# Optimization experiments

Hardware: AMD Instinct MI355X
Metric: run time of the kernel (lower is better)

## Reference

```python
import jax, jax.numpy as jnp
import numpy as np
import math

B, D, E = 32768, 256, 8          # batch, feature dim (shape=[256]), num_steps experts
T_TOTAL = 1.0
H_STEP = T_TOTAL / E             # self.h
EIGMIN, EIGINIT, EIGMAX = -1.0, 0.0, 1.0
LOGIT_099 = math.log(0.99 / 0.01)


def setup_inputs() -> dict:
    key = jax.random.key(0)
    k_t, k_y, k_w1, k_w2 = jax.random.split(key, 4)
    std = 1.0 / math.sqrt(D)     # xavier-ish init for expert weights
    return {
        "t": jax.random.uniform(k_t, (B,), dtype=jnp.float32),            # times in [0, T)
        "y": jax.random.normal(k_y, (B, D), dtype=jnp.float32),
        "W1": jax.random.normal(k_w1, (E, D, D), dtype=jnp.float32) * std,
        "b1": jnp.zeros((E, D), dtype=jnp.float32),
        "W2": jax.random.normal(k_w2, (E, D, D), dtype=jnp.float32) * std,
        "b2": jnp.zeros((E, D), dtype=jnp.float32),
        "scales": jnp.full((1, D), LOGIT_099, dtype=jnp.float32),         # learn_scales=False init
        "shifta": jnp.asarray(LOGIT_099, dtype=jnp.float32),
        "shiftb": jnp.asarray(LOGIT_099, dtype=jnp.float32),
    }


def reference(t, y, W1, b1, W2, b2, scales, shifta, shiftb):
    # t2ind: clamp(int(t / h), max=E-1)
    ind = jnp.minimum((t / H_STEP).astype(jnp.int32), E - 1)            # [B]
    # per-sample dispatch to expert F[i] (2-layer MLP), grouped as masked
    # dense batched GEMMs per expert (E is a small fixed set)
    f = jnp.zeros_like(y)
    for e in range(E):
        h_e = jnp.tanh(jnp.einsum('bd,kd->bk', y, W1[e]) + b1[e])       # [B, D]
        f_e = jnp.einsum('bd,kd->bk', h_e, W2[e]) + b2[e]               # [B, D]
        f = jnp.where((ind == e)[:, None], f_e, f)
    # sigmoid-scale / affine-combine epilogue
    f = jax.nn.sigmoid(scales) * f
    a = EIGINIT + jax.nn.sigmoid(shifta) * (EIGMIN - EIGINIT)
    b = EIGINIT + jax.nn.sigmoid(shiftb) * (EIGMAX - EIGINIT)
    return 0.5 * ((b - a) * f + (a + b) * y)
```

## Files before the change

kernel.cpp:

```cpp
#include <hip/hip_runtime.h>

#define BATCH 32768
#define DIM   256
#define NEXP  8
#define MT    32
#define STRIDE 264

typedef __bf16 bf16x8 __attribute__((ext_vector_type(8)));
typedef __bf16 bf16x4 __attribute__((ext_vector_type(4)));
typedef float  f32x16 __attribute__((ext_vector_type(16)));

static __device__ __forceinline__ float sigmoid_f(float x) {
    return __builtin_amdgcn_rcpf(1.f + __expf(-x));
}
static __device__ __forceinline__ float tanh_f(float x) {
    return 1.f - 2.f * __builtin_amdgcn_rcpf(__expf(2.f * x) + 1.f);
}

static __device__ __forceinline__ void lds_barrier() {
    asm volatile("s_waitcnt lgkmcnt(0)\n\ts_barrier" ::: "memory");
}

__global__ void prep_kernel(const float* __restrict__ W1, const float* __restrict__ W2,
                            const float* __restrict__ t,
                            bf16x8* __restrict__ W1p, bf16x8* __restrict__ W2p,
                            int* __restrict__ cursor, int* __restrict__ idxb) {
    const int b = blockIdx.x;
    if (b < 256) {
        const int tid = b * 256 + threadIdx.x;
        const int kh  = tid & 1;
        const int ks  = (tid >> 1) & 15;
        const int col = (tid >> 5) & 255;
        const int e   = tid >> 13;
        const long src = (long)tid * 8;
        const float4 a0 = *(const float4*)(W1 + src);
        const float4 a1 = *(const float4*)(W1 + src + 4);
        const float4 c0 = *(const float4*)(W2 + src);
        const float4 c1 = *(const float4*)(W2 + src + 4);
        bf16x8 w1, w2;
        w1[0] = (__bf16)a0.x; w1[1] = (__bf16)a0.y; w1[2] = (__bf16)a0.z; w1[3] = (__bf16)a0.w;
        w1[4] = (__bf16)a1.x; w1[5] = (__bf16)a1.y; w1[6] = (__bf16)a1.z; w1[7] = (__bf16)a1.w;
        w2[0] = (__bf16)c0.x; w2[1] = (__bf16)c0.y; w2[2] = (__bf16)c0.z; w2[3] = (__bf16)c0.w;
        w2[4] = (__bf16)c1.x; w2[5] = (__bf16)c1.y; w2[6] = (__bf16)c1.z; w2[7] = (__bf16)c1.w;
        const int dst = (e << 13) | ((col >> 5) << 10) | (ks << 6) | (kh << 5) | (col & 31);
        W1p[dst] = w1;
        W2p[dst] = w2;
    } else {
        __shared__ int h[NEXP], base[NEXP];
        if (threadIdx.x < NEXP) h[threadIdx.x] = 0;
        __syncthreads();
        const int i = (b - 256) * 256 + threadIdx.x;
        const int e = min((int)(t[i] * 8.0f), NEXP - 1);
        const int lr = atomicAdd(&h[e], 1);
        __syncthreads();
        if (threadIdx.x < NEXP)
            base[threadIdx.x] = atomicAdd(&cursor[threadIdx.x], h[threadIdx.x]);
        __syncthreads();
        idxb[e * BATCH + base[e] + lr] = i;
    }
}

__global__ void __launch_bounds__(512, 2)
mlp_kernel(const float* __restrict__ y,
           const float* __restrict__ scales,
           const float* __restrict__ shifta,
           const float* __restrict__ shiftb,
           const float* __restrict__ b1,
           const float* __restrict__ b2,
           const bf16x8* __restrict__ W1p,
           const bf16x8* __restrict__ W2p,
           const int* __restrict__ cnt,
           const int* __restrict__ idxb,
           float* __restrict__ out) {
    __shared__ __bf16 Y[2][MT * STRIDE];
    __shared__ __bf16 H[2][MT * STRIDE];
    __shared__ int rowsb[4][MT];

    const int tx   = threadIdx.x;
    const int wave = tx >> 6;
    const int lane = tx & 63;
    const int nl   = lane & 31;
    const int kh   = lane >> 5;
    const bool isG1 = (wave < 4);
    const int  w    = wave & 3;
    const int  n0   = w * 64 + nl;
    const int  n1   = n0 + 32;

    const int e    = blockIdx.x >> 5;
    const int slot = blockIdx.x & 31;
    const int ce   = cnt[e];
    const int nt_e = (ce + MT - 1) >> 5;
    if (slot >= nt_e) return;
    const int nt   = ((nt_e - slot) + 31) >> 5;
    const int* idx_e = idxb + e * BATCH;

    const bf16x8* wp = (isG1 ? W1p : W2p) + (e << 13) + ((w * 2) << 10) + lane;
    bf16x8 wf[2][16];
#pragma unroll
    for (int s = 0; s < 2; ++s)
#pragma unroll
        for (int ks = 0; ks < 16; ++ks)
            wf[s][ks] = wp[(s << 10) + (ks << 6)];

    const float sa = sigmoid_f(shifta[0]);
    const float sb = sigmoid_f(shiftb[0]);
    const float k1 = 0.5f * (sb + sa);
    const float k2 = 0.5f * (sb - sa);
    const bool needy = (k2 != 0.0f);
    float b1v[2], b2v[2], cc[2];
    b1v[0] = b1[(e << 8) | n0]; b1v[1] = b1[(e << 8) | n1];
    b2v[0] = b2[(e << 8) | n0]; b2v[1] = b2[(e << 8) | n1];
    cc[0]  = k1 * sigmoid_f(scales[n0]); cc[1] = k1 * sigmoid_f(scales[n1]);

    if (!isG1) {
        const int rbase = slot * MT;
        const int nr = min(MT, ce - rbase);
#pragma unroll
        for (int p = 0; p < 8; ++p) {
            const int r  = w * 8 + p;
            const int rr = min(r, nr - 1);
            const int g  = idx_e[rbase + rr];
            if (lane == 0) rowsb[0][r] = (r < nr) ? g : -1;
            const float4 v = *(const float4*)(y + (long)g * DIM + lane * 4);
            bf16x4 wv;
            wv[0] = (__bf16)v.x; wv[1] = (__bf16)v.y; wv[2] = (__bf16)v.z; wv[3] = (__bf16)v.w;
            *(bf16x4*)(&Y[0][r * STRIDE + lane * 4]) = wv;
        }
    }
    lds_barrier();

    for (int t = 0; t <= nt; ++t) {
        if (isG1) {
            if (t < nt) {
                const __bf16* ap = &Y[t & 1][nl * STRIDE + kh * 8];
                f32x16 a0v = {}, a1v = {};
#pragma unroll
                for (int ks = 0; ks < 16; ++ks) {
                    bf16x8 a = *(const bf16x8*)(ap + ks * 16);
                    a0v = __builtin_amdgcn_mfma_f32_32x32x16_bf16(a, wf[0][ks], a0v, 0, 0, 0);
                    a1v = __builtin_amdgcn_mfma_f32_32x32x16_bf16(a, wf[1][ks], a1v, 0, 0, 0);
                }
                __bf16* hb = &H[t & 1][0];
#pragma unroll
                for (int r = 0; r < 16; ++r) {
                    const int row = (r & 3) + ((r >> 2) << 3) + (kh << 2);
                    hb[row * STRIDE + n0] = (__bf16)tanh_f(a0v[r] + b1v[0]);
                    hb[row * STRIDE + n1] = (__bf16)tanh_f(a1v[r] + b1v[1]);
                }
            }
        } else {
            const bool do_stage = (t + 1 < nt);
            int gs[8]; float4 vs[8]; int nr2 = 0;
            if (do_stage) {
                const int rbase = (slot + (t + 1) * 32) * MT;
                nr2 = min(MT, ce - rbase);
#pragma unroll
                for (int p = 0; p < 8; ++p) {
                    const int r  = w * 8 + p;
                    const int rr = min(r, nr2 - 1);
                    gs[p] = idx_e[rbase + rr];
                }
#pragma unroll
                for (int p = 0; p < 8; ++p)
                    vs[p] = *(const float4*)(y + (long)gs[p] * DIM + lane * 4);
            }
            if (t >= 1) {
                const __bf16* ap = &H[(t - 1) & 1][nl * STRIDE + kh * 8];
                f32x16 a0v = {}, a1v = {};
#pragma unroll
                for (int ks = 0; ks < 16; ++ks) {
                    bf16x8 a = *(const bf16x8*)(ap + ks * 16);
                    a0v = __builtin_amdgcn_mfma_f32_32x32x16_bf16(a, wf[0][ks], a0v, 0, 0, 0);
                    a1v = __builtin_amdgcn_mfma_f32_32x32x16_bf16(a, wf[1][ks], a1v, 0, 0, 0);
                }
                const int* rb = rowsb[(t - 1) & 3];
#pragma unroll
                for (int r = 0; r < 16; ++r) {
                    const int row = (r & 3) + ((r >> 2) << 3) + (kh << 2);
                    const int g = rb[row];
                    if (g >= 0) {
                        float r0 = cc[0] * (a0v[r] + b2v[0]);
                        float r1 = cc[1] * (a1v[r] + b2v[1]);
                        if (needy) {
                            r0 += k2 * y[(long)g * DIM + n0];
                            r1 += k2 * y[(long)g * DIM + n1];
                        }
                        out[(long)g * DIM + n0] = r0;
                        out[(long)g * DIM + n1] = r1;
                    }
                }
            }
            if (do_stage) {
                const int kb = t + 1;
#pragma unroll
                for (int p = 0; p < 8; ++p) {
                    const int r = w * 8 + p;
                    if (lane == 0) rowsb[kb & 3][r] = (r < nr2) ? gs[p] : -1;
                    const float4 v = vs[p];
                    bf16x4 wv;
                    wv[0] = (__bf16)v.x; wv[1] = (__bf16)v.y; wv[2] = (__bf16)v.z; wv[3] = (__bf16)v.w;
                    *(bf16x4*)(&Y[kb & 1][r * STRIDE + lane * 4]) = wv;
                }
            }
        }
        lds_barrier();
    }
}

extern "C" void kernel_launch(void* const* d_in, const int* in_sizes, int n_in,
                              void* d_out, int out_size, void* d_ws, size_t ws_size,
                              hipStream_t stream) {
    const float* t      = (const float*)d_in[0];
    const float* y      = (const float*)d_in[1];
    const float* W1     = (const float*)d_in[2];
    const float* b1     = (const float*)d_in[3];
    const float* W2     = (const float*)d_in[4];
    const float* b2     = (const float*)d_in[5];
    const float* scales = (const float*)d_in[6];
    const float* shifta = (const float*)d_in[7];
    const float* shiftb = (const float*)d_in[8];
    float* out = (float*)d_out;

    char* ws = (char*)d_ws;
    int* cursor = (int*)ws;
    int* idxb   = (int*)(ws + 256);
    bf16x8* W1p = (bf16x8*)(ws + 256 + NEXP * BATCH * 4);
    bf16x8* W2p = W1p + 65536;

    hipMemsetAsync(cursor, 0, 32, stream);
    prep_kernel<<<384, 256, 0, stream>>>(W1, W2, t, W1p, W2p, cursor, idxb);
    mlp_kernel<<<256, 512, 0, stream>>>(y, scales, shifta, shiftb, b1, b2,
                                        W1p, W2p, cursor, idxb, out);
}
```

Measured before the change: 122.6 us.

## Replace global atomic bucketing with per-segment counts and in-block LDS compaction

Each prep block now writes its local bucket counts and indices into fixed per-segment slots instead of reserving space with global atomics. That removes the memset of the cursor array and the cross-block atomic contention. Each MLP block then prefix-sums the 128 segment counts and compacts the expert's row indices into an LDS array. Later loads of row indices read from LDS rather than global memory, and the per-tile rowsb table is gone. The trade-offs are a serial prefix loop and a serial copy loop at block start, more LDS use, and a fixed capacity of 5120 rows per expert: rows beyond that cap would be silently dropped.

Measured after the change: 122.6 us. Within noise of the previous version (-0.0%).

```diff
diff --git a/kernel.cpp b/kernel.cpp
--- a/kernel.cpp
+++ b/kernel.cpp
@@ -5,6 +5,7 @@
 #define NEXP  8
 #define MT    32
 #define STRIDE 264
+#define FCAP  5120
 
 typedef __bf16 bf16x8 __attribute__((ext_vector_type(8)));
 typedef __bf16 bf16x4 __attribute__((ext_vector_type(4)));
@@ -24,7 +25,7 @@
 __global__ void prep_kernel(const float* __restrict__ W1, const float* __restrict__ W2,
                             const float* __restrict__ t,
                             bf16x8* __restrict__ W1p, bf16x8* __restrict__ W2p,
-                            int* __restrict__ cursor, int* __restrict__ idxb) {
+                            int* __restrict__ cnts, int* __restrict__ idxb) {
     const int b = blockIdx.x;
     if (b < 256) {
         const int tid = b * 256 + threadIdx.x;
@@ -46,17 +47,17 @@
         W1p[dst] = w1;
         W2p[dst] = w2;
     } else {
-        __shared__ int h[NEXP], base[NEXP];
+        __shared__ int h[NEXP];
+        const int sbid = b - 256;
         if (threadIdx.x < NEXP) h[threadIdx.x] = 0;
         __syncthreads();
-        const int i = (b - 256) * 256 + threadIdx.x;
+        const int i = sbid * 256 + threadIdx.x;
         const int e = min((int)(t[i] * 8.0f), NEXP - 1);
         const int lr = atomicAdd(&h[e], 1);
+        idxb[(e << 15) | (sbid << 8) | lr] = i;
         __syncthreads();
         if (threadIdx.x < NEXP)
-            base[threadIdx.x] = atomicAdd(&cursor[threadIdx.x], h[threadIdx.x]);
-        __syncthreads();
-        idxb[e * BATCH + base[e] + lr] = i;
+            cnts[(threadIdx.x << 7) | sbid] = h[threadIdx.x];
     }
 }
 
@@ -69,12 +70,13 @@
            const float* __restrict__ b2,
            const bf16x8* __restrict__ W1p,
            const bf16x8* __restrict__ W2p,
-           const int* __restrict__ cnt,
+           const int* __restrict__ cnts,
            const int* __restrict__ idxb,
            float* __restrict__ out) {
     __shared__ __bf16 Y[2][MT * STRIDE];
     __shared__ __bf16 H[2][MT * STRIDE];
-    __shared__ int rowsb[4][MT];
+    __shared__ int seg[128];
+    __shared__ int flat[FCAP];
 
     const int tx   = threadIdx.x;
     const int wave = tx >> 6;
@@ -88,11 +90,21 @@
 
     const int e    = blockIdx.x >> 5;
     const int slot = blockIdx.x & 31;
-    const int ce   = cnt[e];
+
+    if (tx < 128) seg[tx] = cnts[(e << 7) | tx];
+    lds_barrier();
+
+    int ce = 0, base = 0;
+#pragma unroll 8
+    for (int j = 0; j < 128; ++j) {
+        if (j == tx) base = ce;
+        ce += seg[j];
+    }
+    ce = min(ce, FCAP);
+
     const int nt_e = (ce + MT - 1) >> 5;
     if (slot >= nt_e) return;
-    const int nt   = ((nt_e - slot) + 31) >> 5;
-    const int* idx_e = idxb + e * BATCH;
+    const int nt = ((nt_e - slot) + 31) >> 5;
 
     const bf16x8* wp = (isG1 ? W1p : W2p) + (e << 13) + ((w * 2) << 10) + lane;
     bf16x8 wf[2][16];
@@ -101,6 +113,15 @@
 #pragma unroll
         for (int ks = 0; ks < 16; ++ks)
             wf[s][ks] = wp[(s << 10) + (ks << 6)];
+
+    if (tx < 128) {
+        const int c = seg[tx];
+        const int* src = idxb + (e << 15) + (tx << 8);
+        for (int j = 0; j < c; ++j) {
+            const int d = base + j;
+            if (d < FCAP) flat[d] = src[j];
+        }
+    }
 
     const float sa = sigmoid_f(shifta[0]);
     const float sb = sigmoid_f(shiftb[0]);
@@ -112,15 +133,14 @@
     b2v[0] = b2[(e << 8) | n0]; b2v[1] = b2[(e << 8) | n1];
     cc[0]  = k1 * sigmoid_f(scales[n0]); cc[1] = k1 * sigmoid_f(scales[n1]);
 
+    lds_barrier();
+
     if (!isG1) {
         const int rbase = slot * MT;
-        const int nr = min(MT, ce - rbase);
 #pragma unroll
         for (int p = 0; p < 8; ++p) {
-            const int r  = w * 8 + p;
-            const int rr = min(r, nr - 1);
-            const int g  = idx_e[rbase + rr];
-            if (lane == 0) rowsb[0][r] = (r < nr) ? g : -1;
+            const int r = w * 8 + p;
+            const int g = flat[min(rbase + r, ce - 1)];
             const float4 v = *(const float4*)(y + (long)g * DIM + lane * 4);
             bf16x4 wv;
             wv[0] = (__bf16)v.x; wv[1] = (__bf16)v.y; wv[2] = (__bf16)v.z; wv[3] = (__bf16)v.w;
@@ -150,19 +170,14 @@
             }
         } else {
             const bool do_stage = (t + 1 < nt);
-            int gs[8]; float4 vs[8]; int nr2 = 0;
+            float4 vs[8];
             if (do_stage) {
                 const int rbase = (slot + (t + 1) * 32) * MT;
-                nr2 = min(MT, ce - rbase);
 #pragma unroll
                 for (int p = 0; p < 8; ++p) {
-                    const int r  = w * 8 + p;
-                    const int rr = min(r, nr2 - 1);
-                    gs[p] = idx_e[rbase + rr];
-                }
-#pragma unroll
-                for (int p = 0; p < 8; ++p)
-                    vs[p] = *(const float4*)(y + (long)gs[p] * DIM + lane * 4);
+                    const int g = flat[min(rbase + w * 8 + p, ce - 1)];
+                    vs[p] = *(const float4*)(y + (long)g * DIM + lane * 4);
+                }
             }
             if (t >= 1) {
                 const __bf16* ap = &H[(t - 1) & 1][nl * STRIDE + kh * 8];
@@ -173,12 +188,13 @@
                     a0v = __builtin_amdgcn_mfma_f32_32x32x16_bf16(a, wf[0][ks], a0v, 0, 0, 0);
                     a1v = __builtin_amdgcn_mfma_f32_32x32x16_bf16(a, wf[1][ks], a1v, 0, 0, 0);
                 }
-                const int* rb = rowsb[(t - 1) & 3];
+                const int rbase = (slot + (t - 1) * 32) * MT;
 #pragma unroll
                 for (int r = 0; r < 16; ++r) {
                     const int row = (r & 3) + ((r >> 2) << 3) + (kh << 2);
-                    const int g = rb[row];
-                    if (g >= 0) {
+                    const int q = rbase + row;
+                    if (q < ce) {
+                        const int g = flat[q];
                         float r0 = cc[0] * (a0v[r] + b2v[0]);
                         float r1 = cc[1] * (a1v[r] + b2v[1]);
                         if (needy) {
@@ -195,7 +211,6 @@
 #pragma unroll
                 for (int p = 0; p < 8; ++p) {
                     const int r = w * 8 + p;
-                    if (lane == 0) rowsb[kb & 3][r] = (r < nr2) ? gs[p] : -1;
                     const float4 v = vs[p];
                     bf16x4 wv;
                     wv[0] = (__bf16)v.x; wv[1] = (__bf16)v.y; wv[2] = (__bf16)v.z; wv[3] = (__bf16)v.w;
@@ -222,13 +237,12 @@
     float* out = (float*)d_out;
 
     char* ws = (char*)d_ws;
-    int* cursor = (int*)ws;
-    int* idxb   = (int*)(ws + 256);
-    bf16x8* W1p = (bf16x8*)(ws + 256 + NEXP * BATCH * 4);
+    int* cnts   = (int*)ws;
+    int* idxb   = (int*)(ws + 4096);
+    bf16x8* W1p = (bf16x8*)(ws + 4096 + NEXP * BATCH * 4);
     bf16x8* W2p = W1p + 65536;
 
-    hipMemsetAsync(cursor, 0, 32, stream);
-    prep_kernel<<<384, 256, 0, stream>>>(W1, W2, t, W1p, W2p, cursor, idxb);
+    prep_kernel<<<384, 256, 0, stream>>>(W1, W2, t, W1p, W2p, cnts, idxb);
     mlp_kernel<<<256, 512, 0, stream>>>(y, scales, shifta, shiftb, b1, b2,
-                                        W1p, W2p, cursor, idxb, out);
-}
+                                        W1p, W2p, cnts, idxb, out);
+}
```

## Prefetch gather indices one tile ahead and move first-tile staging to GEMM1 waves

Applied to the files above, without the earlier changes.

The initial Y tile gather and bf16 staging move from the GEMM2 waves to the GEMM1 waves. Those waves issue the y loads before their weight fragment loads so the two latencies overlap. The index lookups for the gathered rows are now software-pipelined one extra iteration ahead, which takes the dependent idx load off the critical path of the y gather. MFMA loops are wrapped in s_setprio to favour matrix issue; this costs extra registers for the carried indices and rebalances staging work between the wave groups.

After: 120.4 us. No clear change (-1.8%).

```diff
diff --git a/kernel.cpp b/kernel.cpp
--- a/kernel.cpp
+++ b/kernel.cpp
@@ -96,11 +96,45 @@
 
     const bf16x8* wp = (isG1 ? W1p : W2p) + (e << 13) + ((w * 2) << 10) + lane;
     bf16x8 wf[2][16];
-#pragma unroll
-    for (int s = 0; s < 2; ++s)
-#pragma unroll
-        for (int ks = 0; ks < 16; ++ks)
-            wf[s][ks] = wp[(s << 10) + (ks << 6)];
+    int gcur[8];
+
+    if (isG1) {
+        const int rbase = slot * MT;
+        int g0[8];
+#pragma unroll
+        for (int p = 0; p < 8; ++p)
+            g0[p] = idx_e[min(rbase + w * 8 + p, ce - 1)];
+        float4 v0[8];
+#pragma unroll
+        for (int p = 0; p < 8; ++p)
+            v0[p] = *(const float4*)(y + (long)g0[p] * DIM + lane * 4);
+#pragma unroll
+        for (int s = 0; s < 2; ++s)
+#pragma unroll
+            for (int ks = 0; ks < 16; ++ks)
+                wf[s][ks] = wp[(s << 10) + (ks << 6)];
+#pragma unroll
+        for (int p = 0; p < 8; ++p) {
+            const int r = w * 8 + p;
+            if (lane == 0) rowsb[0][r] = (rbase + r < ce) ? g0[p] : -1;
+            const float4 v = v0[p];
+            bf16x4 wv;
+            wv[0] = (__bf16)v.x; wv[1] = (__bf16)v.y; wv[2] = (__bf16)v.z; wv[3] = (__bf16)v.w;
+            *(bf16x4*)(&Y[0][r * STRIDE + lane * 4]) = wv;
+        }
+    } else {
+#pragma unroll
+        for (int s = 0; s < 2; ++s)
+#pragma unroll
+            for (int ks = 0; ks < 16; ++ks)
+                wf[s][ks] = wp[(s << 10) + (ks << 6)];
+        if (nt > 1) {
+            const int rb1 = (slot + 32) * MT;
+#pragma unroll
+            for (int p = 0; p < 8; ++p)
+                gcur[p] = idx_e[min(rb1 + w * 8 + p, ce - 1)];
+        }
+    }
 
     const float sa = sigmoid_f(shifta[0]);
     const float sb = sigmoid_f(shiftb[0]);
@@ -112,21 +146,6 @@
     b2v[0] = b2[(e << 8) | n0]; b2v[1] = b2[(e << 8) | n1];
     cc[0]  = k1 * sigmoid_f(scales[n0]); cc[1] = k1 * sigmoid_f(scales[n1]);
 
-    if (!isG1) {
-        const int rbase = slot * MT;
-        const int nr = min(MT, ce - rbase);
-#pragma unroll
-        for (int p = 0; p < 8; ++p) {
-            const int r  = w * 8 + p;
-            const int rr = min(r, nr - 1);
-            const int g  = idx_e[rbase + rr];
-            if (lane == 0) rowsb[0][r] = (r < nr) ? g : -1;
-            const float4 v = *(const float4*)(y + (long)g * DIM + lane * 4);
-            bf16x4 wv;
-            wv[0] = (__bf16)v.x; wv[1] = (__bf16)v.y; wv[2] = (__bf16)v.z; wv[3] = (__bf16)v.w;
-            *(bf16x4*)(&Y[0][r * STRIDE + lane * 4]) = wv;
-        }
-    }
     lds_barrier();
 
     for (int t = 0; t <= nt; ++t) {
@@ -134,12 +153,14 @@
             if (t < nt) {
                 const __bf16* ap = &Y[t & 1][nl * STRIDE + kh * 8];
                 f32x16 a0v = {}, a1v = {};
+                __builtin_amdgcn_s_setprio(1);
 #pragma unroll
                 for (int ks = 0; ks < 16; ++ks) {
                     bf16x8 a = *(const bf16x8*)(ap + ks * 16);
                     a0v = __builtin_amdgcn_mfma_f32_32x32x16_bf16(a, wf[0][ks], a0v, 0, 0, 0);
                     a1v = __builtin_amdgcn_mfma_f32_32x32x16_bf16(a, wf[1][ks], a1v, 0, 0, 0);
                 }
+                __builtin_amdgcn_s_setprio(0);
                 __bf16* hb = &H[t & 1][0];
 #pragma unroll
                 for (int r = 0; r < 16; ++r) {
@@ -149,30 +170,31 @@
                 }
             }
         } else {
+            int gnew[8];
+            if (t + 2 < nt) {
+                const int rb = (slot + (t + 2) * 32) * MT;
+#pragma unroll
+                for (int p = 0; p < 8; ++p)
+                    gnew[p] = idx_e[min(rb + w * 8 + p, ce - 1)];
+            }
             const bool do_stage = (t + 1 < nt);
-            int gs[8]; float4 vs[8]; int nr2 = 0;
+            float4 vs[8];
             if (do_stage) {
-                const int rbase = (slot + (t + 1) * 32) * MT;
-                nr2 = min(MT, ce - rbase);
-#pragma unroll
-                for (int p = 0; p < 8; ++p) {
-                    const int r  = w * 8 + p;
-                    const int rr = min(r, nr2 - 1);
-                    gs[p] = idx_e[rbase + rr];
-                }
 #pragma unroll
                 for (int p = 0; p < 8; ++p)
-                    vs[p] = *(const float4*)(y + (long)gs[p] * DIM + lane * 4);
+                    vs[p] = *(const float4*)(y + (long)gcur[p] * DIM + lane * 4);
             }
             if (t >= 1) {
                 const __bf16* ap = &H[(t - 1) & 1][nl * STRIDE + kh * 8];
                 f32x16 a0v = {}, a1v = {};
+                __builtin_amdgcn_s_setprio(1);
 #pragma unroll
                 for (int ks = 0; ks < 16; ++ks) {
                     bf16x8 a = *(const bf16x8*)(ap + ks * 16);
                     a0v = __builtin_amdgcn_mfma_f32_32x32x16_bf16(a, wf[0][ks], a0v, 0, 0, 0);
                     a1v = __builtin_amdgcn_mfma_f32_32x32x16_bf16(a, wf[1][ks], a1v, 0, 0, 0);
                 }
+                __builtin_amdgcn_s_setprio(0);
                 const int* rb = rowsb[(t - 1) & 3];
 #pragma unroll
                 for (int r = 0; r < 16; ++r) {
@@ -192,15 +214,18 @@
             }
             if (do_stage) {
                 const int kb = t + 1;
+                const int rbs = (slot + kb * 32) * MT;
 #pragma unroll
                 for (int p = 0; p < 8; ++p) {
                     const int r = w * 8 + p;
-                    if (lane == 0) rowsb[kb & 3][r] = (r < nr2) ? gs[p] : -1;
+                    if (lane == 0) rowsb[kb & 3][r] = (rbs + r < ce) ? gcur[p] : -1;
                     const float4 v = vs[p];
                     bf16x4 wv;
                     wv[0] = (__bf16)v.x; wv[1] = (__bf16)v.y; wv[2] = (__bf16)v.z; wv[3] = (__bf16)v.w;
                     *(bf16x4*)(&Y[kb & 1][r * STRIDE + lane * 4]) = wv;
                 }
+#pragma unroll
+                for (int p = 0; p < 8; ++p) gcur[p] = gnew[p];
             }
         }
         lds_barrier();
```
